# Performance work log

Measured on AMD Instinct MI355X. Metric: run time of the kernel, lower is better.

Reference implementation:

```python
import jax, jax.numpy as jnp
import numpy as np

# module hyperparameters (init_kwargs); topk=-1 is unused by forward
DILATION, SUBSIZE, ANGLE = 4, 16, 4
FLT_MAX = float(np.finfo(np.float32).max)


def _rot_grid(h, w, angle_deg):
    # cv2.warpAffine with M = cv2.getRotationMatrix2D((w/2, h/2), angle, 1)
    # samples the SOURCE at the inverse rotation (rotate dst coords by +angle
    # about the center used by the module, which is (w/2, h/2), not (w-1)/2).
    cx, cy = w / 2.0, h / 2.0
    t = np.deg2rad(angle_deg)
    ca, sa = np.cos(t), np.sin(t)
    xs, ys = np.meshgrid(np.arange(w, dtype=np.float32), np.arange(h, dtype=np.float32))
    sx = ca * xs - sa * ys + (1.0 - ca) * cx + sa * cy
    sy = sa * xs + ca * ys - sa * cx + (1.0 - ca) * cy
    return jnp.asarray(sx, jnp.float32), jnp.asarray(sy, jnp.float32)


def _bilinear(img, sx, sy):
    # img [..., H, W]; bilinear sample with zero border (cv2 BORDER_CONSTANT)
    H, W = img.shape[-2], img.shape[-1]
    x0f, y0f = jnp.floor(sx), jnp.floor(sy)
    wx1, wy1 = sx - x0f, sy - y0f
    wx0, wy0 = 1.0 - wx1, 1.0 - wy1
    x0, y0 = x0f.astype(jnp.int32), y0f.astype(jnp.int32)

    def gather(xi, yi):
        valid = ((xi >= 0) & (xi < W) & (yi >= 0) & (yi < H)).astype(img.dtype)
        v = img[..., jnp.clip(yi, 0, H - 1), jnp.clip(xi, 0, W - 1)]
        return v * valid

    return (wy0 * wx0 * gather(x0, y0) + wy0 * wx1 * gather(x0 + 1, y0)
            + wy1 * wx0 * gather(x0, y0 + 1) + wy1 * wx1 * gather(x0 + 1, y0 + 1))


def _forward(fm1, fm2):
    bs, c, h, w = fm1.shape  # module assumes c == 1 (squeezes channel dim)
    d = min(h, w, DILATION)
    ss = min(h, w, SUBSIZE)
    fm2 = jax.lax.stop_gradient(fm2)  # torch detaches ref2 before warpAffine
    grids = [_rot_grid(ss, ss, a) for a in range(-ANGLE, ANGLE + 1)]
    # rotated validity mask (warped all-ones image), same for every block
    masks = [_bilinear(jnp.ones((ss, ss), fm1.dtype), gx, gy) for gx, gy in grids]
    total = jnp.zeros((bs,), fm1.dtype)
    for sub_x in range(0, w, ss):
        for sub_y in range(0, h, ss):
            r1 = fm1[:, 0, sub_y:sub_y + ss, sub_x:sub_x + ss]  # [bs,ss,ss]
            # the nested border-case slicing is exactly a clamp of the start index
            starts = [(int(np.clip(sub_y + dh, 0, h - ss)), int(np.clip(sub_x + dw, 0, w - ss)))
                      for dw in range(-d, d + 1) for dh in range(-d, d + 1)]
            blocks = jnp.stack([fm2[:, 0, y0:y0 + ss, x0:x0 + ss] for (y0, x0) in starts])  # [S,bs,ss,ss]
            sub_min = jnp.full((bs,), FLT_MAX, fm1.dtype)
            for (gx, gy), m in zip(grids, masks):
                r_blocks = _bilinear(blocks, gx, gy)        # [S,bs,ss,ss] rotated candidates
                se = (r1[None] - r_blocks) ** 2 * m          # masked squared error
                rands = se.sum((-1, -2)) / m.sum()           # [S,bs] rotate_mse_loss
                sub_min = jnp.minimum(sub_min, rands.min(0))
            total = total + sub_min
    return total


def setup_inputs():
    key = jax.random.key(0)
    k1, k2 = jax.random.split(key)
    fm1 = jax.random.normal(k1, (1024, 1, 64, 64), jnp.float32)
    fm2 = jax.random.normal(k2, (1024, 1, 64, 64), jnp.float32)
    return {"fm1": fm1, "fm2": fm2}


def reference(fm1, fm2):
    return _forward(fm1, fm2)
```

## Files before the change

### kernel.cpp

```cpp
#include <hip/hip_runtime.h>
#include <hip/hip_fp16.h>
#include <math.h>

#define NANG 9
#define SS 16
#define NPIX 256
#define WSH 72
#define NROWW 70
#define WINSZH (NROWW * WSH)
#define NITEM (NANG * 16)
#define NWAVE 8
#define IPW (NITEM / NWAVE)
#define FLTMAX_BITS 0x7F7FFFFFu


__global__ __launch_bounds__(256) void build_table(uint4* __restrict__ tbl)
{
    __shared__ float red[256];
    const int p  = threadIdx.x;
    const int px = p & 15, py = p >> 4;
    for (int a = 0; a < NANG; ++a) {
        double t  = (double)(a - 4) * 0.017453292519943295;
        double ca = cos(t), sa = sin(t);
        float sx = (float)(ca * px - sa * py + (1.0 - ca) * 8.0 + sa * 8.0);
        float sy = (float)(sa * px + ca * py - sa * 8.0 + (1.0 - ca) * 8.0);
        float x0f = floorf(sx), y0f = floorf(sy);
        int   x0  = (int)x0f,   y0  = (int)y0f;
        float wx1 = sx - x0f, wx0 = 1.0f - wx1;
        float wy1 = sy - y0f, wy0 = 1.0f - wy1;
        float ewx0 = (x0 >= 0 && x0 < SS)         ? wx0 : 0.0f;
        float ewx1 = (x0 + 1 >= 0 && x0 + 1 < SS) ? wx1 : 0.0f;
        float ewy0 = (y0 >= 0 && y0 < SS)         ? wy0 : 0.0f;
        float ewy1 = (y0 + 1 >= 0 && y0 + 1 < SS) ? wy1 : 0.0f;
        float m = (ewx0 + ewx1) * (ewy0 + ewy1);

        red[p] = m;
        __syncthreads();
        for (int s = 128; s > 0; s >>= 1) {
            if (p < s) red[p] += red[p + s];
            __syncthreads();
        }
        float msum = red[0];
        __syncthreads();

        float sc = sqrtf(m / msum);
        x0 = max(-1, min(15, x0));
        y0 = max(-1, min(15, y0));
        uint4 e;
        e.x = (unsigned)__half_as_ushort(__float2half(ewx0)) |
              ((unsigned)__half_as_ushort(__float2half(ewx1)) << 16);
        e.y = (unsigned)__half_as_ushort(__float2half(-sc * ewy0)) |
              ((unsigned)__half_as_ushort(__float2half(-sc * ewy1)) << 16);
        e.z = __float_as_uint(sc);
        e.w = (unsigned)((y0 + 1) * WSH + (x0 + 1));
        tbl[a * NPIX + p] = e;
    }
}

#define DPPADD(v, ctrl, rmask)                                                   \
    v += __int_as_float(__builtin_amdgcn_update_dpp(                             \
            0, __float_as_int(v), ctrl, rmask, 0xf, true))

template<int NP>
__device__ __forceinline__ void rowload(const __half2* __restrict__ winh,
                                        int (&addr)[4],
                                        const __half2 (&wx0)[4], const __half2 (&wx1)[4],
                                        __half2 (&h)[4][NP])
{
    #pragma unroll
    for (int k = 0; k < 4; ++k) {
        __half2 d[2 * NP];
        #pragma unroll
        for (int j = 0; j < 2 * NP; ++j) d[j] = winh[addr[k] + j];
        #pragma unroll
        for (int c = 0; c < NP; ++c)
            h[k][c] = __hfma2(wx1[k], d[2 * c + 1], __hmul2(wx0[k], d[2 * c]));
        addr[k] += WSH;
    }
}

template<int NP>
__device__ __forceinline__ void bystep(const __half2 (&hp)[4][NP], const __half2 (&hc)[4][NP],
                                       const __half2 (&wy0n)[4], const __half2 (&wy1n)[4],
                                       const __half2 (&r1s)[4],
                                       unsigned* __restrict__ sm, int lane)
{
    __half2 acc[NP];
    #pragma unroll
    for (int c = 0; c < NP; ++c) acc[c] = __floats2half2_rn(0.f, 0.f);
    #pragma unroll
    for (int k = 0; k < 4; ++k) {
        #pragma unroll
        for (int c = 0; c < NP; ++c) {
            __half2 e = __hfma2(wy0n[k], hp[k][c], r1s[k]);
            e = __hfma2(wy1n[k], hc[k][c], e);
            acc[c] = __hfma2(e, e, acc[c]);
        }
    }
    constexpr int NJ = 2 * NP - 1;
    float v[NJ];
    #pragma unroll
    for (int c = 0; c < NP; ++c) {
        v[2 * c] = __low2float(acc[c]);
        if (2 * c + 1 < NJ) v[2 * c + 1] = __high2float(acc[c]);
    }
    #pragma unroll
    for (int j = 0; j < NJ; ++j) {
        DPPADD(v[j], 0xB1,  0xf);
        DPPADD(v[j], 0x4E,  0xf);
        DPPADD(v[j], 0x141, 0xf);
        DPPADD(v[j], 0x140, 0xf);
        DPPADD(v[j], 0x142, 0xa);
        DPPADD(v[j], 0x143, 0xc);
    }
    if (lane == 63) {
        float best = v[0];
        #pragma unroll
        for (int j = 1; j < NJ; ++j) best = fminf(best, v[j]);
        atomicMin(sm, __float_as_uint(best));
    }
}

template<int NBY, int NP>
__device__ __forceinline__ void proc(const __half2* __restrict__ winh, int (&addr)[4],
                                     const __half2 (&wx0)[4], const __half2 (&wx1)[4],
                                     const __half2 (&wy0n)[4], const __half2 (&wy1n)[4],
                                     const __half2 (&r1s)[4],
                                     unsigned* __restrict__ sm, int lane)
{
    __half2 hA[4][NP], hB[4][NP];
    rowload<NP>(winh, addr, wx0, wx1, hA);
    #pragma unroll
    for (int by = 0; by < NBY + 1; by += 2) {
        rowload<NP>(winh, addr, wx0, wx1, hB);
        bystep<NP>(hA, hB, wy0n, wy1n, r1s, sm, lane);
        if (by + 1 < NBY + 1) {
            rowload<NP>(winh, addr, wx0, wx1, hA);
            bystep<NP>(hB, hA, wy0n, wy1n, r1s, sm, lane);
        }
    }
}

__global__ __launch_bounds__(512) void randip_main(const float* __restrict__ fm1,
                                                   const float* __restrict__ fm2,
                                                   const uint4* __restrict__ gt,
                                                   float* __restrict__ out)
{
    __shared__ __half2 winh[WINSZH];
    __shared__ unsigned submin[16];

    const int b    = blockIdx.x;
    const int tid  = threadIdx.x;
    const int wave = tid >> 6;
    const int lane = tid & 63;

    for (int i = tid; i < WINSZH; i += 512) winh[i] = __floats2half2_rn(0.f, 0.f);
    if (tid < 16) submin[tid] = FLTMAX_BITS;
    __syncthreads();

    const float* img2 = fm2 + (size_t)b * 4096;
    for (int i = tid; i < 64 * 65; i += 512) {
        int r = i / 65, c = i - r * 65;
        float lo = (c >= 1)  ? img2[r * 64 + c - 1] : 0.f;
        float hi = (c <= 63) ? img2[r * 64 + c]     : 0.f;
        winh[(r + 1) * WSH + c] = __floats2half2_rn(lo, hi);
    }
    __syncthreads();

    const float* img1 = fm1 + (size_t)b * 4096;

    int a_cur = -1;
    __half2 wx0[4], wx1[4], wy0n[4], wy1n[4], r1s[4];
    float   sca[4];
    int     off[4];

    for (int i = wave * IPW; i < (wave + 1) * IPW; ++i) {
        const int a = i >> 4, sub = i & 15;
        if (a != a_cur) {
            a_cur = a;
            const uint4* tp = gt + a * NPIX + lane;
            #pragma unroll
            for (int k = 0; k < 4; ++k) {
                uint4 te = tp[64 * k];
                __half2 X = *(const __half2*)&te.x;
                __half2 Y = *(const __half2*)&te.y;
                wx0[k]  = __half2half2(__low2half(X));
                wx1[k]  = __half2half2(__high2half(X));
                wy0n[k] = __half2half2(__low2half(Y));
                wy1n[k] = __half2half2(__high2half(Y));
                sca[k]  = __uint_as_float(te.z);
                off[k]  = (int)te.w;
            }
        }
        const int sub_x = (sub & 3) << 4;
        const int sub_y = (sub >> 2) << 4;
        const int x_lo = max(sub_x - 4, 0);
        const int y_lo = max(sub_y - 4, 0);
        const int nvx = min(sub_x + 4, 48) - x_lo;
        const int nby = min(sub_y + 4, 48) - y_lo;
        const int rowbase0 = y_lo * WSH + x_lo;

        const float* r1p = img1 + (sub_y + (lane >> 4)) * 64 + sub_x + (lane & 15);
        #pragma unroll
        for (int k = 0; k < 4; ++k)
            r1s[k] = __float2half2_rn(sca[k] * r1p[k * 4 * 64]);

        int addr[4];
        #pragma unroll
        for (int k = 0; k < 4; ++k) addr[k] = rowbase0 + off[k];

        unsigned* sm = &submin[sub];
        if (nby == 8) {
            if (nvx == 8) proc<8, 5>(winh, addr, wx0, wx1, wy0n, wy1n, r1s, sm, lane);
            else          proc<8, 3>(winh, addr, wx0, wx1, wy0n, wy1n, r1s, sm, lane);
        } else {
            if (nvx == 8) proc<4, 5>(winh, addr, wx0, wx1, wy0n, wy1n, r1s, sm, lane);
            else          proc<4, 3>(winh, addr, wx0, wx1, wy0n, wy1n, r1s, sm, lane);
        }
    }
    __syncthreads();

    if (tid == 0) {
        float t = 0.0f;
        #pragma unroll
        for (int s = 0; s < 16; ++s) t += __uint_as_float(submin[s]);
        out[b] = t;
    }
}

extern "C" void kernel_launch(void* const* d_in, const int* in_sizes, int n_in,
                              void* d_out, int out_size, void* d_ws, size_t ws_size,
                              hipStream_t stream)
{
    const float* fm1 = (const float*)d_in[0];
    const float* fm2 = (const float*)d_in[1];
    float* out = (float*)d_out;
    uint4* tbl = (uint4*)d_ws;

    const int nb = in_sizes[0] >> 12;

    hipLaunchKernelGGL(build_table, dim3(1), dim3(256), 0, stream, tbl);
    hipLaunchKernelGGL(randip_main, dim3(nb), dim3(512), 0, stream, fm1, fm2, tbl, out);
}
```

Measured before the change: 351.9 us.

## Permute pixel-to-lane assignment to spread LDS window reads across banks

The table builder now sorts the 256 sampled pixels of each angle by the LDS bank of their window offset (offset mod 32) and stores them in a permuted order, so each lane's four table entries cover pixels that hit distinct banks. The original pixel index is packed into the high bits of the table word, and the main kernel uses it to fetch the matching fm1 pixel. The aim is to cut LDS bank conflicts in the row loads of the bilinear window. In exchange the fm1 loads become scattered rather than coalesced, and the single-block setup kernel does more serial counting work.

```diff
diff --git a/kernel.cpp b/kernel.cpp
--- a/kernel.cpp
+++ b/kernel.cpp
@@ -17,6 +17,10 @@
 __global__ __launch_bounds__(256) void build_table(uint4* __restrict__ tbl)
 {
     __shared__ float red[256];
+    __shared__ unsigned char clsArr[256];
+    __shared__ int H[32];
+    __shared__ int startArr[32];
+
     const int p  = threadIdx.x;
     const int px = p & 15, py = p >> 4;
     for (int a = 0; a < NANG; ++a) {
@@ -46,14 +50,36 @@
         float sc = sqrtf(m / msum);
         x0 = max(-1, min(15, x0));
         y0 = max(-1, min(15, y0));
+        const int off = (y0 + 1) * WSH + (x0 + 1);
         uint4 e;
         e.x = (unsigned)__half_as_ushort(__float2half(ewx0)) |
               ((unsigned)__half_as_ushort(__float2half(ewx1)) << 16);
         e.y = (unsigned)__half_as_ushort(__float2half(-sc * ewy0)) |
               ((unsigned)__half_as_ushort(__float2half(-sc * ewy1)) << 16);
         e.z = __float_as_uint(sc);
-        e.w = (unsigned)((y0 + 1) * WSH + (x0 + 1));
-        tbl[a * NPIX + p] = e;
+        e.w = (unsigned)off | ((unsigned)p << 16);
+
+        const int cls = off & 31;
+        clsArr[p] = (unsigned char)cls;
+        __syncthreads();
+        int rank = 0;
+        for (int q = 0; q < 256; ++q)
+            rank += (clsArr[q] == (unsigned char)cls) && (q < p);
+        if (p < 32) {
+            int h = 0;
+            for (int q = 0; q < 256; ++q) h += (clsArr[q] == (unsigned char)p);
+            H[p] = h;
+        }
+        __syncthreads();
+        if (p == 0) {
+            int acc = 0;
+            for (int c = 0; c < 32; ++c) { startArr[c] = acc; acc += H[c]; }
+        }
+        __syncthreads();
+        const int s    = startArr[cls] + rank;
+        const int nidx = (s & 3) * 64 + (s >> 2);
+        tbl[a * NPIX + nidx] = e;
+        __syncthreads();
     }
 }
 
@@ -172,7 +198,7 @@
     int a_cur = -1;
     __half2 wx0[4], wx1[4], wy0n[4], wy1n[4], r1s[4];
     float   sca[4];
-    int     off[4];
+    int     off[4], o1[4];
 
     for (int i = wave * IPW; i < (wave + 1) * IPW; ++i) {
         const int a = i >> 4, sub = i & 15;
@@ -189,7 +215,9 @@
                 wy0n[k] = __half2half2(__low2half(Y));
                 wy1n[k] = __half2half2(__high2half(Y));
                 sca[k]  = __uint_as_float(te.z);
-                off[k]  = (int)te.w;
+                off[k]  = (int)(te.w & 0xffffu);
+                const int p = (int)(te.w >> 16);
+                o1[k]  = (p >> 4) * 64 + (p & 15);
             }
         }
         const int sub_x = (sub & 3) << 4;
@@ -200,10 +228,10 @@
         const int nby = min(sub_y + 4, 48) - y_lo;
         const int rowbase0 = y_lo * WSH + x_lo;
 
-        const float* r1p = img1 + (sub_y + (lane >> 4)) * 64 + sub_x + (lane & 15);
+        const float* img1sub = img1 + sub_y * 64 + sub_x;
         #pragma unroll
         for (int k = 0; k < 4; ++k)
-            r1s[k] = __float2half2_rn(sca[k] * r1p[k * 4 * 64]);
+            r1s[k] = __float2half2_rn(sca[k] * img1sub[o1[k]]);
 
         int addr[4];
         #pragma unroll
```

After: 432.8 us. 23.0% more time.
